# Performance work log

Hardware: AMD Instinct MI355X
Metric: run time of the kernel (lower is better)

The kernel has to match this reference:

```python
import jax, jax.numpy as jnp
import numpy as np

B, T, C = 1024, 50, 66   # batch, frames, motion dim
H = 1024                 # LSTM state size
EPS = 1e-5               # LN_v2 epsilon


def _lstm_cell(x, h, c, W_ih, W_hh, b):
    # PyTorch gate order: input, forget, cell, output
    g = x @ W_ih.T + h @ W_hh.T + b            # [B, 4H]
    i, f, gg, o = jnp.split(g, 4, axis=-1)
    i = jax.nn.sigmoid(i)
    f = jax.nn.sigmoid(f)
    gg = jnp.tanh(gg)
    o = jax.nn.sigmoid(o)
    c2 = f * c + i * gg
    h2 = o * jnp.tanh(c2)
    return h2, c2


def setup_inputs() -> dict:
    key = jax.random.key(0)
    ks = jax.random.split(key, 12)
    s = 1.0 / np.sqrt(H)  # PyTorch LSTM init range
    return {
        "x": jax.random.normal(ks[0], (B, T, C), jnp.float32),
        # layer 0 (input_size=C); b folds PyTorch b_ih + b_hh (same math)
        "W_ih0": jax.random.uniform(ks[1], (4 * H, C), jnp.float32, -s, s),
        "W_hh0": jax.random.uniform(ks[2], (4 * H, H), jnp.float32, -s, s),
        "b0": jax.random.uniform(ks[3], (4 * H,), jnp.float32, -s, s),
        # layer 1 (input_size=H)
        "W_ih1": jax.random.uniform(ks[4], (4 * H, H), jnp.float32, -s, s),
        "W_hh1": jax.random.uniform(ks[5], (4 * H, H), jnp.float32, -s, s),
        "b1": jax.random.uniform(ks[6], (4 * H,), jnp.float32, -s, s),
        # fc0: xavier with gain 1e-8 -> near-zero weights; small scale here
        "fc_w": jax.random.normal(ks[7], (C, H), jnp.float32) * 1e-3,
        "fc_b": jnp.zeros((C,), jnp.float32),
        # LN_v2 params
        "alpha": jnp.ones((C,), jnp.float32),
        "beta": jnp.zeros((C,), jnp.float32),
    }


def reference(x, W_ih0, W_hh0, b0, W_ih1, W_hh1, b1, fc_w, fc_b, alpha, beta):
    z = jnp.zeros((x.shape[0], H), x.dtype)

    def stack(xt, h0, c0, h1, c1):
        h0, c0 = _lstm_cell(xt, h0, c0, W_ih0, W_hh0, b0)
        h1, c1 = _lstm_cell(h0, h1, c1, W_ih1, W_hh1, b1)
        return h0, c0, h1, c1

    # Encoder: consume x[:, :-1, :], keep final (h, c) of both layers
    def enc_step(carry, xt):
        return stack(xt, *carry), None

    carry, _ = jax.lax.scan(enc_step, (z, z, z, z),
                            jnp.swapaxes(x[:, :-1, :], 0, 1))

    def ln(v):  # LN_v2: layernorm over last dim, learnable alpha/beta
        m = v.mean(-1, keepdims=True)
        var = ((v - m) ** 2).mean(-1, keepdims=True)
        return (v - m) / jnp.sqrt(var + EPS) * alpha + beta

    def dec_step(carry, _):
        h0, c0, h1, c1, dec = carry
        h0, c0, h1, c1 = stack(dec, h0, c0, h1, c1)
        delta = h1 @ fc_w.T + fc_b            # fc0
        new = ln(delta) + dec                 # recursive_residual=True
        return (h0, c0, h1, c1, new), new

    dec0 = x[:, -1, :]
    _, outs = jax.lax.scan(dec_step, carry + (dec0,), None, length=x.shape[1])
    return jnp.swapaxes(outs, 0, 1)           # [B, T, C]
```

## Files before the change

kernel.cpp:

```cpp
#include <hip/hip_runtime.h>
#include <cstdint>
#include <cmath>

typedef unsigned short u16;
typedef unsigned long long u64;
typedef __bf16 v8bf __attribute__((ext_vector_type(8)));
typedef float v4f __attribute__((ext_vector_type(4)));

__device__ __forceinline__ u16 f2bf(float f) {
    unsigned int u = __float_as_uint(f);
    u += 0x7fffu + ((u >> 16) & 1u);
    return (u16)(u >> 16);
}
__device__ __forceinline__ float sigmoidf_(float x) { return 1.0f / (1.0f + __expf(-x)); }
__device__ __forceinline__ float tanhf_(float x) {
    float e = __expf(2.0f * x);
    return 1.0f - 2.0f / (e + 1.0f);
}

#define AGLD(g, l, aux)                                                    \
    __builtin_amdgcn_global_load_lds(                                      \
        (const __attribute__((address_space(1))) unsigned int*)(g),        \
        (__attribute__((address_space(3))) unsigned int*)(l), 16, 0, aux)

__device__ __forceinline__ u64 aload64(const u16* p) {
    return __hip_atomic_load((const u64*)p, __ATOMIC_RELAXED, __HIP_MEMORY_SCOPE_AGENT);
}
__device__ __forceinline__ void astore64(u16* p, u64 v) {
    __hip_atomic_store((u64*)p, v, __ATOMIC_RELAXED, __HIP_MEMORY_SCOPE_AGENT);
}

__device__ __forceinline__ void grid_bar(unsigned* bar, int phase) {
    asm volatile("s_waitcnt vmcnt(0)" ::: "memory");
    __syncthreads();
    if (threadIdx.x == 0) {
        unsigned* leaf = bar + 32 * ((blockIdx.x & 7) + 1);
        unsigned v = __hip_atomic_fetch_add(leaf, 1u, __ATOMIC_RELAXED, __HIP_MEMORY_SCOPE_AGENT);
        if ((v & 31u) == 31u)
            __hip_atomic_fetch_add(bar, 1u, __ATOMIC_RELAXED, __HIP_MEMORY_SCOPE_AGENT);
        const unsigned target = 8u * (unsigned)phase;
        while (__hip_atomic_load(bar, __ATOMIC_RELAXED, __HIP_MEMORY_SCOPE_AGENT) < target)
            __builtin_amdgcn_s_sleep(4);
    }
    __syncthreads();
}

__device__ __forceinline__ void gemm_layer(
    const u16* __restrict__ A1, int K1, int S1, bool a1ro,
    const u16* __restrict__ A2, int S2,
    const u16* __restrict__ W, int Ktot,
    const float* __restrict__ bias,
    float* __restrict__ Cst, u16* __restrict__ Hout,
    int m0, int n0, u16* smem)
{
    const int tid  = threadIdx.x;
    const int wave = tid >> 6;
    const int lane = tid & 63;
    const int l16  = lane & 15;
    const int lq   = lane >> 4;
    const int wrb  = (wave >> 1) * 64;
    const int wcb  = (wave & 1) * 64;

    v4f acc[4][4];
#pragma unroll
    for (int i = 0; i < 4; ++i)
#pragma unroll
        for (int j = 0; j < 4; ++j) acc[i][j] = (v4f){0.f, 0.f, 0.f, 0.f};

    const int srow = tid >> 3;
    const int skc  = tid & 7;

    auto stage_tile = [&](int k0, int buf) {
        u16* At = smem + buf * 16384;
        u16* Bt = At + 8192;
        const u16* src; int kof, st; bool ro;
        if (k0 < K1) { src = A1; kof = k0;      st = S1; ro = a1ro; }
        else         { src = A2; kof = k0 - K1; st = S2; ro = false; }
        if (ro) {
#pragma unroll
            for (int r = 0; r < 4; ++r) {
                int c = tid + r * 256;
                int row = srow + r * 32;
                int kc  = skc ^ (row & 7);
                AGLD(src + (size_t)(m0 + row) * st + kof + kc * 8, At + c * 8, 0);
            }
        } else {
#pragma unroll
            for (int r = 0; r < 4; ++r) {
                int c = tid + r * 256;
                int row = srow + r * 32;
                int kc  = skc ^ (row & 7);
                AGLD(src + (size_t)(m0 + row) * st + kof + kc * 8, At + c * 8, 17);
            }
        }
#pragma unroll
        for (int r = 0; r < 4; ++r) {
            int c = tid + r * 256;
            int row = srow + r * 32;
            int kc  = skc ^ (row & 7);
            AGLD(W + (size_t)(n0 + row) * Ktot + k0 + kc * 8, Bt + c * 8, 0);
        }
    };

    const int nt = Ktot >> 6;
    stage_tile(0, 0);
    for (int it = 0; it < nt; ++it) {
        __syncthreads();
        if (it + 1 < nt) stage_tile((it + 1) << 6, (it + 1) & 1);
        const u16* At = smem + (it & 1) * 16384;
        const u16* Bt = At + 8192;
#pragma unroll
        for (int kk = 0; kk < 64; kk += 32) {
            const int kcb = kk >> 3;
            v8bf a[4], b[4];
#pragma unroll
            for (int mi = 0; mi < 4; ++mi) {
                int row = wrb + mi * 16 + l16;
                int p = row * 8 + ((kcb + lq) ^ (row & 7));
                a[mi] = *(const v8bf*)(At + p * 8);
            }
#pragma unroll
            for (int ni = 0; ni < 4; ++ni) {
                int row = wcb + ni * 16 + l16;
                int p = row * 8 + ((kcb + lq) ^ (row & 7));
                b[ni] = *(const v8bf*)(Bt + p * 8);
            }
#pragma unroll
            for (int mi = 0; mi < 4; ++mi)
#pragma unroll
                for (int ni = 0; ni < 4; ++ni)
                    acc[mi][ni] = __builtin_amdgcn_mfma_f32_16x16x32_bf16(
                        a[mi], b[ni], acc[mi][ni], 0, 0, 0);
        }
    }
    __syncthreads();

    float* gates = (float*)smem;
#pragma unroll
    for (int p = 0; p < 2; ++p) {
        if ((wave >> 1) == p) {
#pragma unroll
            for (int mi = 0; mi < 4; ++mi)
#pragma unroll
                for (int ni = 0; ni < 4; ++ni) {
                    int col = wcb + ni * 16 + l16;
                    float bs = bias[n0 + col];
#pragma unroll
                    for (int r = 0; r < 4; ++r) {
                        int row = mi * 16 + lq * 4 + r;
                        gates[row * 132 + col] = acc[mi][ni][r] + bs;
                    }
                }
        }
        __syncthreads();
#pragma unroll
        for (int j = 0; j < 2; ++j) {
            int it2 = tid + j * 256;
            int row = it2 >> 3, ug = (it2 & 7) * 4;
            const float* gp = gates + row * 132 + ug * 4;
            int b = m0 + p * 64 + row;
            int U = (n0 >> 2) + ug;
            float4 c4 = *(const float4*)(Cst + (size_t)b * 1024 + U);
            u64 hq; u16* hqs = (u16*)&hq;
#pragma unroll
            for (int q = 0; q < 4; ++q) {
                float gi = gp[q * 4 + 0], gf = gp[q * 4 + 1];
                float gg = gp[q * 4 + 2], go = gp[q * 4 + 3];
                float c  = (&c4.x)[q];
                float i_ = sigmoidf_(gi);
                float f_ = sigmoidf_(gf);
                float g_ = tanhf_(gg);
                float o_ = sigmoidf_(go);
                float c2 = f_ * c + i_ * g_;
                (&c4.x)[q] = c2;
                hqs[q] = f2bf(o_ * tanhf_(c2));
            }
            *(float4*)(Cst + (size_t)b * 1024 + U) = c4;
            astore64(Hout + (size_t)b * 1024 + U, hq);
        }
        __syncthreads();
    }
}

__device__ __forceinline__ void fc_ln(
    int blk, const u16* __restrict__ H1, const u16* __restrict__ Wf,
    const float* __restrict__ fcb, const float* __restrict__ alpha,
    const float* __restrict__ beta,
    const float* __restrict__ decprev, float* __restrict__ outp,
    u16* __restrict__ decnext)
{
    const int tid  = threadIdx.x;
    const int wave = tid >> 6, lane = tid & 63;
    const int l16  = lane & 15, lq = lane >> 4;
    const int b0   = blk * 64 + wave * 16;

    v4f acc[5];
#pragma unroll
    for (int i = 0; i < 5; ++i) acc[i] = (v4f){0.f, 0.f, 0.f, 0.f};

    for (int k = 0; k < 1024; k += 32) {
        const u16* ap = H1 + (size_t)(b0 + l16) * 1024 + k + lq * 8;
        union { u64 q[2]; v8bf v; } uu;
        uu.q[0] = aload64(ap);
        uu.q[1] = aload64(ap + 4);
        v8bf a = uu.v;
#pragma unroll
        for (int ni = 0; ni < 5; ++ni) {
            v8bf bb = *(const v8bf*)(Wf + (size_t)(ni * 16 + l16) * 1024 + k + lq * 8);
            acc[ni] = __builtin_amdgcn_mfma_f32_16x16x32_bf16(a, bb, acc[ni], 0, 0, 0);
        }
    }

    float av[5], bv[5], fb[5]; int valid[5];
#pragma unroll
    for (int ni = 0; ni < 5; ++ni) {
        int col = ni * 16 + l16;
        valid[ni] = col < 66;
        fb[ni] = valid[ni] ? fcb[col]   : 0.f;
        av[ni] = valid[ni] ? alpha[col] : 0.f;
        bv[ni] = valid[ni] ? beta[col]  : 0.f;
    }
#pragma unroll
    for (int r = 0; r < 4; ++r) {
        int b = b0 + lq * 4 + r;
        float d[5];
        float s = 0.f;
#pragma unroll
        for (int ni = 0; ni < 5; ++ni) {
            d[ni] = valid[ni] ? (acc[ni][r] + fb[ni]) : 0.f;
            s += d[ni];
        }
#pragma unroll
        for (int m = 1; m < 16; m <<= 1) s += __shfl_xor(s, m, 64);
        float mean = s * (1.f / 66.f);
        float vs = 0.f;
#pragma unroll
        for (int ni = 0; ni < 5; ++ni) {
            float t = valid[ni] ? (d[ni] - mean) : 0.f;
            vs += t * t;
        }
#pragma unroll
        for (int m = 1; m < 16; m <<= 1) vs += __shfl_xor(vs, m, 64);
        float inv = rsqrtf(vs * (1.f / 66.f) + 1e-5f);
#pragma unroll
        for (int ni = 0; ni < 5; ++ni) {
            if (valid[ni]) {
                int col = ni * 16 + l16;
                float y = (d[ni] - mean) * inv * av[ni] + bv[ni]
                        + decprev[(size_t)b * 3300 + col];
                outp[(size_t)b * 3300 + col] = y;
                __hip_atomic_store(decnext + (size_t)b * 128 + col, f2bf(y),
                                   __ATOMIC_RELAXED, __HIP_MEMORY_SCOPE_AGENT);
            }
        }
    }
}

__global__ __launch_bounds__(256)
void lstm_persistent(const u16* __restrict__ Xbuf, u16* __restrict__ DEC,
                     u16* __restrict__ H0, u16* __restrict__ H1,
                     float* __restrict__ C0, float* __restrict__ C1,
                     const u16* __restrict__ Wc0, const u16* __restrict__ Wc1,
                     const float* __restrict__ B0p, const float* __restrict__ B1p,
                     const u16* __restrict__ fcwb, const float* __restrict__ fcb,
                     const float* __restrict__ alpha, const float* __restrict__ beta,
                     const float* __restrict__ x, float* __restrict__ out,
                     unsigned* __restrict__ bar)
{
    __shared__ alignas(16) u16 smem[32768];
    const int blk = blockIdx.x;
    const int m0  = (blk >> 5) * 128;
    const int n0  = (blk & 31) * 128;
    const size_t HSZ = 1024 * 1024;
    int ph = 0;

    gemm_layer(Xbuf, 128, 128, true, H0, 1024, Wc0, 1152, B0p, C0, H0 + HSZ, m0, n0, smem);
    grid_bar(bar, ++ph);
    for (int s = 0; s < 48; ++s) {
        const u16* h0w = H0 + (size_t)((s + 1) & 1) * HSZ;
        gemm_layer(h0w, 1024, 1024, false, H1 + (size_t)(s & 1) * HSZ, 1024,
                   Wc1, 2048, B1p, C1, H1 + (size_t)((s + 1) & 1) * HSZ, m0, n0, smem);
        gemm_layer(Xbuf + (size_t)(s + 1) * (1024 * 128), 128, 128, true, h0w, 1024,
                   Wc0, 1152, B0p, C0, H0 + (size_t)(s & 1) * HSZ, m0, n0, smem);
        grid_bar(bar, ++ph);
    }
    gemm_layer(H0 + HSZ, 1024, 1024, false, H1, 1024,
               Wc1, 2048, B1p, C1, H1 + HSZ, m0, n0, smem);
    grid_bar(bar, ++ph);

    for (int s = 49; s < 99; ++s) {
        int d = s - 49;
        const u16* A1 = DEC + (size_t)(d & 1) * (1024 * 128);
        u16* h0r = H0 + (size_t)(s & 1) * HSZ;
        u16* h0w = H0 + (size_t)((s + 1) & 1) * HSZ;
        u16* h1r = H1 + (size_t)(s & 1) * HSZ;
        u16* h1w = H1 + (size_t)((s + 1) & 1) * HSZ;

        gemm_layer(A1, 128, 128, false, h0r, 1024, Wc0, 1152, B0p, C0, h0w, m0, n0, smem);
        grid_bar(bar, ++ph);
        gemm_layer(h0w, 1024, 1024, false, h1r, 1024, Wc1, 2048, B1p, C1, h1w, m0, n0, smem);
        grid_bar(bar, ++ph);
        if (blk < 16) {
            const float* decprev = (d == 0) ? (x + 49 * 66) : (out + (size_t)(d - 1) * 66);
            fc_ln(blk, h1w, fcwb, fcb, alpha, beta, decprev, out + (size_t)d * 66,
                  DEC + (size_t)((d + 1) & 1) * (1024 * 128));
        }
        grid_bar(bar, ++ph);
    }
}

__global__ void k_init_w0(const float* __restrict__ Wih, const float* __restrict__ Whh,
                          u16* __restrict__ Wc)
{
    int idx = blockIdx.x * 256 + threadIdx.x;
    if (idx >= 4096 * 1152) return;
    int jp = idx / 1152, k = idx - jp * 1152;
    int u = jp >> 2, g = jp & 3;
    float v = 0.f;
    if (k < 66)        v = Wih[(g * 1024 + u) * 66 + k];
    else if (k >= 128) v = Whh[(size_t)(g * 1024 + u) * 1024 + (k - 128)];
    Wc[idx] = f2bf(v);
}
__global__ void k_init_w1(const float* __restrict__ Wih, const float* __restrict__ Whh,
                          u16* __restrict__ Wc)
{
    int idx = blockIdx.x * 256 + threadIdx.x;
    int jp = idx >> 11, k = idx & 2047;
    int u = jp >> 2, g = jp & 3;
    float v = (k < 1024) ? Wih[(size_t)(g * 1024 + u) * 1024 + k]
                         : Whh[(size_t)(g * 1024 + u) * 1024 + (k - 1024)];
    Wc[idx] = f2bf(v);
}
__global__ void k_init_fcw(const float* __restrict__ fcw, u16* __restrict__ Wb)
{
    int idx = blockIdx.x * 256 + threadIdx.x;
    int r = idx >> 10, k = idx & 1023;
    float v = (r < 66) ? fcw[(size_t)r * 1024 + k] : 0.f;
    Wb[idx] = f2bf(v);
}
__global__ void k_init_bias(const float* __restrict__ b0, const float* __restrict__ b1,
                            float* __restrict__ B0p, float* __restrict__ B1p)
{
    int idx = blockIdx.x * 256 + threadIdx.x;
    if (idx < 4096) B0p[idx] = b0[(idx & 3) * 1024 + (idx >> 2)];
    else { int j = idx - 4096; B1p[j] = b1[(j & 3) * 1024 + (j >> 2)]; }
}
__global__ void k_init_x(const float* __restrict__ x, u16* __restrict__ Xbuf,
                         u16* __restrict__ DEC0)
{
    int idx = blockIdx.x * 256 + threadIdx.x;
    int t = idx >> 17;
    int b = (idx >> 7) & 1023;
    int c = idx & 127;
    float v = (c < 66) ? x[(size_t)b * 3300 + t * 66 + c] : 0.f;
    u16 h = f2bf(v);
    if (t < 49) Xbuf[idx] = h;
    else        DEC0[b * 128 + c] = h;
}
__global__ void k_init_state(u16* __restrict__ H0z, u16* __restrict__ H1z,
                             float* __restrict__ C0, float* __restrict__ C1,
                             u16* __restrict__ DEC1, unsigned* __restrict__ bar)
{
    int idx = blockIdx.x * 256 + threadIdx.x;
    H0z[idx] = 0; H1z[idx] = 0;
    C0[idx] = 0.f; C1[idx] = 0.f;
    if (idx < 1024 * 128) DEC1[idx] = 0;
    if (idx < 1024) bar[idx] = 0u;
}

extern "C" void kernel_launch(void* const* d_in, const int* in_sizes, int n_in,
                              void* d_out, int out_size, void* d_ws, size_t ws_size,
                              hipStream_t stream)
{
    const float* x     = (const float*)d_in[0];
    const float* Wih0  = (const float*)d_in[1];
    const float* Whh0  = (const float*)d_in[2];
    const float* b0    = (const float*)d_in[3];
    const float* Wih1  = (const float*)d_in[4];
    const float* Whh1  = (const float*)d_in[5];
    const float* b1    = (const float*)d_in[6];
    const float* fcw   = (const float*)d_in[7];
    const float* fcb   = (const float*)d_in[8];
    const float* alpha = (const float*)d_in[9];
    const float* beta  = (const float*)d_in[10];
    float* out = (float*)d_out;

    char* p = (char*)d_ws;
    auto take = [&](size_t bytes) { char* r = p; p += (bytes + 255) & ~(size_t)255; return r; };
    u16*      Wc0  = (u16*)take((size_t)4096 * 1152 * 2);
    u16*      Wc1  = (u16*)take((size_t)4096 * 2048 * 2);
    u16*      fcwb = (u16*)take((size_t)80 * 1024 * 2);
    float*    B0p  = (float*)take(4096 * 4);
    float*    B1p  = (float*)take(4096 * 4);
    u16*      Xbuf = (u16*)take((size_t)49 * 1024 * 128 * 2);
    u16*      DEC  = (u16*)take((size_t)2 * 1024 * 128 * 2);
    u16*      H0   = (u16*)take((size_t)2 * 1024 * 1024 * 2);
    u16*      H1   = (u16*)take((size_t)2 * 1024 * 1024 * 2);
    float*    C0   = (float*)take((size_t)1024 * 1024 * 4);
    float*    C1   = (float*)take((size_t)1024 * 1024 * 4);
    unsigned* bar  = (unsigned*)take(4096);

    k_init_w0<<<18432, 256, 0, stream>>>(Wih0, Whh0, Wc0);
    k_init_w1<<<32768, 256, 0, stream>>>(Wih1, Whh1, Wc1);
    k_init_fcw<<<320, 256, 0, stream>>>(fcw, fcwb);
    k_init_bias<<<32, 256, 0, stream>>>(b0, b1, B0p, B1p);
    k_init_x<<<25600, 256, 0, stream>>>(x, Xbuf, DEC);
    k_init_state<<<4096, 256, 0, stream>>>(H0, H1, C0, C1, DEC + 1024 * 128, bar);

    lstm_persistent<<<dim3(256), 256, 0, stream>>>(
        Xbuf, DEC, H0, H1, C0, C1, Wc0, Wc1, B0p, B1p,
        fcwb, fcb, alpha, beta, x, out, bar);
}
```

Before: 6.731 ms.

## Keep LSTM cell state in registers and change Xbuf load cache policy

The LSTM cell-state arrays C0/C1, previously read and written in global memory at every step, now live in per-thread register arrays inside the persistent kernel. This works because each thread always owns the same (batch, unit) elements across steps. The read-only input loads switch from aux 0 to cache-policy aux 2, passed through an int parameter in place of a bool. This removes 8 MB of global traffic per step and the state zero-initialisation, at the cost of extra registers, which could raise pressure or cause spills in the 4x4 accumulator GEMM.

```diff
diff --git a/kernel.cpp b/kernel.cpp
--- a/kernel.cpp
+++ b/kernel.cpp
@@ -46,11 +46,12 @@
 }
 
 __device__ __forceinline__ void gemm_layer(
-    const u16* __restrict__ A1, int K1, int S1, bool a1ro,
+    const u16* __restrict__ A1, int K1, int S1, int a1aux,
     const u16* __restrict__ A2, int S2,
     const u16* __restrict__ W, int Ktot,
     const float* __restrict__ bias,
-    float* __restrict__ Cst, u16* __restrict__ Hout,
+    float* __restrict__ cst,
+    u16* __restrict__ Hout,
     int m0, int n0, u16* smem)
 {
     const int tid  = threadIdx.x;
@@ -73,24 +74,24 @@
     auto stage_tile = [&](int k0, int buf) {
         u16* At = smem + buf * 16384;
         u16* Bt = At + 8192;
-        const u16* src; int kof, st; bool ro;
-        if (k0 < K1) { src = A1; kof = k0;      st = S1; ro = a1ro; }
-        else         { src = A2; kof = k0 - K1; st = S2; ro = false; }
-        if (ro) {
-#pragma unroll
-            for (int r = 0; r < 4; ++r) {
-                int c = tid + r * 256;
-                int row = srow + r * 32;
-                int kc  = skc ^ (row & 7);
-                AGLD(src + (size_t)(m0 + row) * st + kof + kc * 8, At + c * 8, 0);
-            }
-        } else {
+        const u16* src; int kof, st, aux;
+        if (k0 < K1) { src = A1; kof = k0;      st = S1; aux = a1aux; }
+        else         { src = A2; kof = k0 - K1; st = S2; aux = 17; }
+        if (aux == 17) {
 #pragma unroll
             for (int r = 0; r < 4; ++r) {
                 int c = tid + r * 256;
                 int row = srow + r * 32;
                 int kc  = skc ^ (row & 7);
                 AGLD(src + (size_t)(m0 + row) * st + kof + kc * 8, At + c * 8, 17);
+            }
+        } else if (aux == 2) {
+#pragma unroll
+            for (int r = 0; r < 4; ++r) {
+                int c = tid + r * 256;
+                int row = srow + r * 32;
+                int kc  = skc ^ (row & 7);
+                AGLD(src + (size_t)(m0 + row) * st + kof + kc * 8, At + c * 8, 2);
             }
         }
 #pragma unroll
@@ -160,22 +161,20 @@
             const float* gp = gates + row * 132 + ug * 4;
             int b = m0 + p * 64 + row;
             int U = (n0 >> 2) + ug;
-            float4 c4 = *(const float4*)(Cst + (size_t)b * 1024 + U);
+            float* cs = cst + (p * 2 + j) * 4;
             u64 hq; u16* hqs = (u16*)&hq;
 #pragma unroll
             for (int q = 0; q < 4; ++q) {
                 float gi = gp[q * 4 + 0], gf = gp[q * 4 + 1];
                 float gg = gp[q * 4 + 2], go = gp[q * 4 + 3];
-                float c  = (&c4.x)[q];
                 float i_ = sigmoidf_(gi);
                 float f_ = sigmoidf_(gf);
                 float g_ = tanhf_(gg);
                 float o_ = sigmoidf_(go);
-                float c2 = f_ * c + i_ * g_;
-                (&c4.x)[q] = c2;
+                float c2 = f_ * cs[q] + i_ * g_;
+                cs[q] = c2;
                 hqs[q] = f2bf(o_ * tanhf_(c2));
             }
-            *(float4*)(Cst + (size_t)b * 1024 + U) = c4;
             astore64(Hout + (size_t)b * 1024 + U, hq);
         }
         __syncthreads();
@@ -259,7 +258,6 @@
 __global__ __launch_bounds__(256)
 void lstm_persistent(const u16* __restrict__ Xbuf, u16* __restrict__ DEC,
                      u16* __restrict__ H0, u16* __restrict__ H1,
-                     float* __restrict__ C0, float* __restrict__ C1,
                      const u16* __restrict__ Wc0, const u16* __restrict__ Wc1,
                      const float* __restrict__ B0p, const float* __restrict__ B1p,
                      const u16* __restrict__ fcwb, const float* __restrict__ fcb,
@@ -274,18 +272,22 @@
     const size_t HSZ = 1024 * 1024;
     int ph = 0;
 
-    gemm_layer(Xbuf, 128, 128, true, H0, 1024, Wc0, 1152, B0p, C0, H0 + HSZ, m0, n0, smem);
+    float c0s[16], c1s[16];
+#pragma unroll
+    for (int i = 0; i < 16; ++i) { c0s[i] = 0.f; c1s[i] = 0.f; }
+
+    gemm_layer(Xbuf, 128, 128, 2, H0, 1024, Wc0, 1152, B0p, c0s, H0 + HSZ, m0, n0, smem);
     grid_bar(bar, ++ph);
     for (int s = 0; s < 48; ++s) {
         const u16* h0w = H0 + (size_t)((s + 1) & 1) * HSZ;
-        gemm_layer(h0w, 1024, 1024, false, H1 + (size_t)(s & 1) * HSZ, 1024,
-                   Wc1, 2048, B1p, C1, H1 + (size_t)((s + 1) & 1) * HSZ, m0, n0, smem);
-        gemm_layer(Xbuf + (size_t)(s + 1) * (1024 * 128), 128, 128, true, h0w, 1024,
-                   Wc0, 1152, B0p, C0, H0 + (size_t)(s & 1) * HSZ, m0, n0, smem);
+        gemm_layer(h0w, 1024, 1024, 17, H1 + (size_t)(s & 1) * HSZ, 1024,
+                   Wc1, 2048, B1p, c1s, H1 + (size_t)((s + 1) & 1) * HSZ, m0, n0, smem);
+        gemm_layer(Xbuf + (size_t)(s + 1) * (1024 * 128), 128, 128, 2, h0w, 1024,
+                   Wc0, 1152, B0p, c0s, H0 + (size_t)(s & 1) * HSZ, m0, n0, smem);
         grid_bar(bar, ++ph);
     }
-    gemm_layer(H0 + HSZ, 1024, 1024, false, H1, 1024,
-               Wc1, 2048, B1p, C1, H1 + HSZ, m0, n0, smem);
+    gemm_layer(H0 + HSZ, 1024, 1024, 17, H1, 1024,
+               Wc1, 2048, B1p, c1s, H1 + HSZ, m0, n0, smem);
     grid_bar(bar, ++ph);
 
     for (int s = 49; s < 99; ++s) {
@@ -296,9 +298,9 @@
         u16* h1r = H1 + (size_t)(s & 1) * HSZ;
         u16* h1w = H1 + (size_t)((s + 1) & 1) * HSZ;
 
-        gemm_layer(A1, 128, 128, false, h0r, 1024, Wc0, 1152, B0p, C0, h0w, m0, n0, smem);
+        gemm_layer(A1, 128, 128, 17, h0r, 1024, Wc0, 1152, B0p, c0s, h0w, m0, n0, smem);
         grid_bar(bar, ++ph);
-        gemm_layer(h0w, 1024, 1024, false, h1r, 1024, Wc1, 2048, B1p, C1, h1w, m0, n0, smem);
+        gemm_layer(h0w, 1024, 1024, 17, h1r, 1024, Wc1, 2048, B1p, c1s, h1w, m0, n0, smem);
         grid_bar(bar, ++ph);
         if (blk < 16) {
             const float* decprev = (d == 0) ? (x + 49 * 66) : (out + (size_t)(d - 1) * 66);
@@ -358,12 +360,10 @@
     else        DEC0[b * 128 + c] = h;
 }
 __global__ void k_init_state(u16* __restrict__ H0z, u16* __restrict__ H1z,
-                             float* __restrict__ C0, float* __restrict__ C1,
                              u16* __restrict__ DEC1, unsigned* __restrict__ bar)
 {
     int idx = blockIdx.x * 256 + threadIdx.x;
     H0z[idx] = 0; H1z[idx] = 0;
-    C0[idx] = 0.f; C1[idx] = 0.f;
     if (idx < 1024 * 128) DEC1[idx] = 0;
     if (idx < 1024) bar[idx] = 0u;
 }
@@ -396,8 +396,6 @@
     u16*      DEC  = (u16*)take((size_t)2 * 1024 * 128 * 2);
     u16*      H0   = (u16*)take((size_t)2 * 1024 * 1024 * 2);
     u16*      H1   = (u16*)take((size_t)2 * 1024 * 1024 * 2);
-    float*    C0   = (float*)take((size_t)1024 * 1024 * 4);
-    float*    C1   = (float*)take((size_t)1024 * 1024 * 4);
     unsigned* bar  = (unsigned*)take(4096);
 
     k_init_w0<<<18432, 256, 0, stream>>>(Wih0, Whh0, Wc0);
@@ -405,9 +403,9 @@
     k_init_fcw<<<320, 256, 0, stream>>>(fcw, fcwb);
     k_init_bias<<<32, 256, 0, stream>>>(b0, b1, B0p, B1p);
     k_init_x<<<25600, 256, 0, stream>>>(x, Xbuf, DEC);
-    k_init_state<<<4096, 256, 0, stream>>>(H0, H1, C0, C1, DEC + 1024 * 128, bar);
+    k_init_state<<<4096, 256, 0, stream>>>(H0, H1, DEC + 1024 * 128, bar);
 
     lstm_persistent<<<dim3(256), 256, 0, stream>>>(
-        Xbuf, DEC, H0, H1, C0, C1, Wc0, Wc1, B0p, B1p,
+        Xbuf, DEC, H0, H1, Wc0, Wc1, B0p, B1p,
         fcwb, fcb, alpha, beta, x, out, bar);
 }
```

Result: slower. 7.065 ms (+5.0%).
